# Performance work log

Measured on AMD Instinct MI355X. Metric: run time of the kernel, lower is better.

## Reference

```python
import jax, jax.numpy as jnp
import numpy as np

COST_CLASS = 1.0
COST_L1 = 1.0


def _lsa(cost):
    """Exact rectangular linear sum assignment (Jonker-Volgenant / e-maxx Hungarian).
    cost: (n, m) numpy float64 with n <= m. Returns ans[n]: column assigned to each row.
    """
    n, m = cost.shape
    INF = np.inf
    u = np.zeros(n + 1)
    v = np.zeros(m + 1)
    p = np.zeros(m + 1, dtype=np.int64)    # p[j]: 1-indexed row matched to column j (0 = free)
    way = np.zeros(m + 1, dtype=np.int64)
    for i in range(1, n + 1):
        p[0] = i
        j0 = 0
        minv = np.full(m + 1, INF)
        used = np.zeros(m + 1, dtype=bool)
        while True:
            used[j0] = True
            i0 = p[j0]
            minv1 = minv[1:]               # view, in-place updates propagate
            jmask = ~used[1:]
            cur = cost[i0 - 1, :] - u[i0] - v[1:]
            upd = jmask & (cur < minv1)
            minv1[upd] = cur[upd]
            way[1:][upd] = j0
            idx = np.nonzero(jmask)[0]
            j1rel = idx[np.argmin(minv1[idx])]
            delta = minv1[j1rel]
            u[p[used]] += delta
            v[used] -= delta
            minv1[jmask] -= delta
            j0 = j1rel + 1
            if p[j0] == 0:
                break
        # augment along the alternating path
        while j0:
            j1 = way[j0]
            p[j0] = p[j1]
            j0 = j1
    ans = np.zeros(n, dtype=np.int64)
    for j in range(1, m + 1):
        if p[j] > 0:
            ans[p[j] - 1] = j - 1
    return ans


def _solve_blocks(blocks):
    """blocks: (B, Q, T) numpy. Per-batch optimal assignment, scipy-compatible output:
    row_ind sorted ascending, min(Q,T) pairs (here Q >= T so T pairs)."""
    blocks = np.asarray(blocks, dtype=np.float64)
    B, Q, T = blocks.shape
    rows = np.empty((B, T), dtype=np.int32)
    cols = np.empty((B, T), dtype=np.int32)
    for b in range(B):
        c = blocks[b]
        if Q >= T:
            ans = _lsa(c.T)                      # ans[t] = matched query q
            order = np.argsort(ans, kind="stable")
            rows[b] = ans[order]
            cols[b] = order
        else:
            ans = _lsa(c)
            rows[b] = np.arange(Q)
            cols[b] = ans
    return rows, cols


def _cost_blocks(outputs, targets):
    """Diagonal (per-sample) blocks of the DETR cost matrix.
    outputs: (B, Q, 1+P); targets: (B, T, 1+P). Returns (B, Q, T).
    Math identical to building the full (B*Q, B*T) matrix and slicing, as in the source."""
    out_prob = jax.nn.softmax(outputs[:, :, 0], axis=-1)      # softmax over the QUERY axis (as in source)
    out_pos = outputs[:, :, 1:]                                # (B, Q, P)
    tgt_pos = targets[:, :, 1:]                                # (B, T, P)
    cost_l1 = jnp.abs(out_pos[:, :, None, :] - tgt_pos[:, None, :, :]).sum(-1)  # L1 cdist, (B, Q, T)
    return COST_CLASS * (-out_prob[:, :, None]) + COST_L1 * cost_l1


def setup_inputs() -> dict:
    key = jax.random.key(0)
    k1, k2 = jax.random.split(key)
    outputs = jax.random.normal(k1, (8, 2048, 3), dtype=jnp.float32)
    targets = jax.random.uniform(k2, (8, 256, 3), dtype=jnp.float32)
    return {"outputs": outputs, "targets": targets}


def reference(outputs, targets):
    blocks = _cost_blocks(outputs, targets)                    # (B, Q, T)
    B, Q, T = blocks.shape
    n = min(Q, T)
    shapes = (jax.ShapeDtypeStruct((B, n), jnp.int32),
              jax.ShapeDtypeStruct((B, n), jnp.int32))
    row_ind, col_ind = jax.pure_callback(_solve_blocks, shapes, blocks)
    return row_ind, col_ind
```

## Files before the change

### kernel.cpp

```cpp
#include <hip/hip_runtime.h>


constexpr int B = 8;
constexpr int Q = 2048;
constexpr int T = 256;
constexpr int NT = 256;
constexpr int KPT = Q / NT;
constexpr int NW = NT / 64;

struct __align__(16) CD { double u; float tx, ty; };

__device__ __forceinline__ unsigned wave_min_u32_dpp(unsigned a) {
  int v = (int)a, t;
  t = __builtin_amdgcn_update_dpp(v, v, 0x111, 0xf, 0xf, false);
  v = ((unsigned)t < (unsigned)v) ? t : v;
  t = __builtin_amdgcn_update_dpp(v, v, 0x112, 0xf, 0xf, false);
  v = ((unsigned)t < (unsigned)v) ? t : v;
  t = __builtin_amdgcn_update_dpp(v, v, 0x114, 0xf, 0xf, false);
  v = ((unsigned)t < (unsigned)v) ? t : v;
  t = __builtin_amdgcn_update_dpp(v, v, 0x118, 0xf, 0xf, false);
  v = ((unsigned)t < (unsigned)v) ? t : v;
  t = __builtin_amdgcn_update_dpp(v, v, 0x142, 0xf, 0xf, false);
  v = ((unsigned)t < (unsigned)v) ? t : v;
  t = __builtin_amdgcn_update_dpp(v, v, 0x143, 0xf, 0xf, false);
  v = ((unsigned)t < (unsigned)v) ? t : v;
  return (unsigned)__builtin_amdgcn_readlane(v, 63);
}

__launch_bounds__(NT, 1)
__global__ void hungarian_r14(const float* __restrict__ outs,
                              const float* __restrict__ tgts,
                              int* __restrict__ out) {
  const int b = blockIdx.x;
  const int tid = threadIdx.x;
  const int lane = tid & 63;
  const int wv = tid >> 6;

  __shared__ CD colDat[Q + 1];
  __shared__ float2 rowTgt[T + 1];
  __shared__ short p[Q + 1];
  __shared__ uint4 pk2[2][NW][2];
  __shared__ double vdelta[Q];
  __shared__ int ansArr[T];
  __shared__ double s_rv[NW];
  __shared__ float sh_f;

  const size_t qbase = (size_t)b * Q;
  const size_t tbase = (size_t)b * T;

  float xs[KPT], qx[KPT], qy[KPT];
#pragma unroll
  for (int k = 0; k < KPT; ++k) {
    const size_t o = (qbase + tid + k * NT) * 3;
    xs[k] = outs[o];
    qx[k] = outs[o + 1];
    qy[k] = outs[o + 2];
  }
  {
    const size_t o = (tbase + tid) * 3;
    rowTgt[tid + 1] = make_float2(tgts[o + 1], tgts[o + 2]);
    if (tid == 0) rowTgt[0] = make_float2(0.f, 0.f);
  }

  float lmax = xs[0];
#pragma unroll
  for (int k = 1; k < KPT; ++k) lmax = fmaxf(lmax, xs[k]);
  for (int off = 32; off > 0; off >>= 1) lmax = fmaxf(lmax, __shfl_down(lmax, off));
  if ((tid & 63) == 0) s_rv[tid >> 6] = (double)lmax;
  __syncthreads();
  if (tid == 0) {
    float m2 = (float)s_rv[0];
    for (int w = 1; w < NW; ++w) m2 = fmaxf(m2, (float)s_rv[w]);
    sh_f = m2;
  }
  __syncthreads();
  const float smax = sh_f;
  float ex[KPT];
  float lsum = 0.f;
#pragma unroll
  for (int k = 0; k < KPT; ++k) { ex[k] = expf(xs[k] - smax); lsum += ex[k]; }
  for (int off = 32; off > 0; off >>= 1) lsum += __shfl_down(lsum, off);
  if ((tid & 63) == 0) s_rv[tid >> 6] = (double)lsum;
  __syncthreads();
  if (tid == 0) {
    float s2 = 0.f;
    for (int w = 0; w < NW; ++w) s2 += (float)s_rv[w];
    sh_f = s2;
  }
  __syncthreads();
  const float ssum = sh_f;
  float np_[KPT];
#pragma unroll
  for (int k = 0; k < KPT; ++k) np_[k] = -(ex[k] / ssum);

  for (int j = tid; j <= Q; j += NT) {
    p[j] = 0;
    CD c0; c0.u = 0.0; c0.tx = -1.0f; c0.ty = 0.0f;
    colDat[j] = c0;
  }
  double vreg[KPT];
#pragma unroll
  for (int k = 0; k < KPT; ++k) {
    vreg[k] = 0.0;
    vdelta[tid + (k << 8)] = 0.0;
  }
  __syncthreads();

  const float FINF = __int_as_float(0x7f800000);
  float2 nxtT = rowTgt[1];

  for (int i = 1; i <= T; ++i) {
    unsigned usedMask = 0;
    double D = 0.0;
    int i0 = i;
    double ui0 = 0.0;
    float tX = nxtT.x, tY = nxtT.y;
    int s = 0, S;
    int j1v = 0;
    int recRow = 0, recCol = 0, recPrev = 0;
    double recU = 0.0, recD = 0.0;
    float recTX = 0.f, recTY = 0.f;

    for (;;) {
      if (tid == s) {
        recRow = i0; recU = ui0; recTX = tX; recTY = tY; recD = D; recPrev = j1v;
      }

      double cv[KPT];
#pragma unroll
      for (int k = 0; k < KPT; ++k) {
        float cf = fabsf(qx[k] - tX) + fabsf(qy[k] - tY) + np_[k];
        if (usedMask & (1u << k)) cf = FINF;
        cv[k] = ((double)cf - ui0) - vreg[k];
      }
      const double m01 = fmin(cv[0], cv[1]), m23 = fmin(cv[2], cv[3]);
      const double m45 = fmin(cv[4], cv[5]), m67 = fmin(cv[6], cv[7]);
      const double m03 = fmin(m01, m23), m47 = fmin(m45, m67);
      double bval = fmin(m03, m47);
      unsigned emsk = 0;
#pragma unroll
      for (int k = 0; k < KPT; ++k) emsk |= (cv[k] == bval) ? (1u << k) : 0u;
      const int bk = (int)__builtin_ctz(emsk);
      int bidx = 1 + tid + (bk << 8);

      const CD myCd = colDat[bidx];

      bval += 0.0;
      const long long bb = __double_as_longlong(bval);
      const unsigned long long key = (unsigned long long)bb ^
          ((bb < 0) ? 0xFFFFFFFFFFFFFFFFull : 0x8000000000000000ull);
      const unsigned khi = (unsigned)(key >> 32);
      const unsigned klo = (unsigned)key;

      const unsigned minhi = wave_min_u32_dpp(khi);
      const unsigned long long mask = __ballot(khi == minhi);
      int wl;
      if (__popcll(mask) == 1) {
        wl = (int)__ffsll(mask) - 1;
      } else {
        unsigned wklo = 0xffffffffu; int widx = 0x7fffffff; wl = 0;
        unsigned long long mm = mask;
        while (mm) {
          const int l = (int)__ffsll(mm) - 1; mm &= mm - 1;
          const unsigned lo2 = (unsigned)__builtin_amdgcn_readlane((int)klo, l);
          const int ix2 = __builtin_amdgcn_readlane(bidx, l);
          if (lo2 < wklo || (lo2 == wklo && ix2 < widx)) {
            wklo = lo2; widx = ix2; wl = l;
          }
        }
      }
      const int par = s & 1;
      if (lane == wl) {
        pk2[par][wv][0] = make_uint4(minhi, klo, (unsigned)bidx, 0u);
        const unsigned long long cu =
            (unsigned long long)__double_as_longlong(myCd.u);
        pk2[par][wv][1] = make_uint4((unsigned)cu, (unsigned)(cu >> 32),
                                     __float_as_uint(myCd.tx),
                                     __float_as_uint(myCd.ty));
      }
      __syncthreads();

      const uint4 c0v = pk2[par][0][0];
      const uint4 c1v = pk2[par][1][0];
      const uint4 c2v = pk2[par][2][0];
      const uint4 c3v = pk2[par][3][0];
      const uint4 d0v = pk2[par][0][1];
      const uint4 d1v = pk2[par][1][1];
      const uint4 d2v = pk2[par][2][1];
      const uint4 d3v = pk2[par][3][1];

      const unsigned long long k0b = ((unsigned long long)c0v.x << 32) | c0v.y;
      const unsigned long long k1b = ((unsigned long long)c1v.x << 32) | c1v.y;
      const unsigned long long k2b = ((unsigned long long)c2v.x << 32) | c2v.y;
      const unsigned long long k3b = ((unsigned long long)c3v.x << 32) | c3v.y;
      const int j0b = (int)c0v.z, j1bb = (int)c1v.z;
      const int j2b = (int)c2v.z, j3b = (int)c3v.z;
      const bool w01 = (k1b < k0b) || (k1b == k0b && j1bb < j0b);
      const unsigned long long k01 = w01 ? k1b : k0b;
      const int j01 = w01 ? j1bb : j0b;
      const bool w23 = (k3b < k2b) || (k3b == k2b && j3b < j2b);
      const unsigned long long k23 = w23 ? k3b : k2b;
      const int j23 = w23 ? j3b : j2b;
      const bool wf = (k23 < k01) || (k23 == k01 && j23 < j01);
      const unsigned long long bkk = wf ? k23 : k01;
      const int j1 = wf ? j23 : j01;
      const unsigned ulA = w01 ? d1v.x : d0v.x, uhA = w01 ? d1v.y : d0v.y;
      const unsigned xAf = w01 ? d1v.z : d0v.z, yAf = w01 ? d1v.w : d0v.w;
      const unsigned ulB = w23 ? d3v.x : d2v.x, uhB = w23 ? d3v.y : d2v.y;
      const unsigned xBf = w23 ? d3v.z : d2v.z, yBf = w23 ? d3v.w : d2v.w;
      const unsigned ulW = wf ? ulB : ulA, uhW = wf ? uhB : uhA;
      const unsigned xW = wf ? xBf : xAf, yW = wf ? yBf : yAf;
      const double cdun = __longlong_as_double(
          (long long)(((unsigned long long)uhW << 32) | ulW));
      const float cdtx = __uint_as_float(xW);
      const float cdty = __uint_as_float(yW);

      const long long db = (long long)((bkk & 0x8000000000000000ull)
                                           ? (bkk ^ 0x8000000000000000ull) : ~bkk);
      D += __longlong_as_double(db);
      if (tid == ((j1 - 1) & 255)) usedMask |= 1u << ((j1 - 1) >> 8);
      if (tid == s) recCol = j1;
      const int pj1 = (int)p[j1];
      j1v = j1;
      ++s;
      if (cdtx < 0.0f) { S = s; break; }
      ui0 = cdun; tX = cdtx; tY = cdty; i0 = pj1;
    }

    __syncthreads();
    nxtT = rowTgt[i < T ? i + 1 : T];
    const double Dfin = D;
    if (tid < S) {
      p[recCol] = (short)recRow;
      const double unew = recU + (Dfin - recD);
      CD c2; c2.u = unew; c2.tx = recTX; c2.ty = recTY;
      colDat[recCol] = c2;
      if (tid >= 1) {
        vdelta[recPrev - 1] = Dfin - recD;
      }
    }
    __syncthreads();
#pragma unroll
    for (int k = 0; k < KPT; ++k) {
      const double dv = vdelta[tid + (k << 8)];
      vreg[k] -= dv;
      vdelta[tid + (k << 8)] = 0.0;
    }
  }
  __syncthreads();

  for (int j = 1 + tid; j <= Q; j += NT) {
    const int pi = (int)p[j];
    if (pi > 0) ansArr[pi - 1] = j - 1;
  }
  __syncthreads();
  const int a = ansArr[tid];
  int rank = 0;
  for (int t2 = 0; t2 < T; ++t2) rank += (ansArr[t2] < a) ? 1 : 0;
  out[(size_t)b * T + rank] = a;
  out[(size_t)B * T + (size_t)b * T + rank] = tid;
}

extern "C" void kernel_launch(void* const* d_in, const int* in_sizes, int n_in,
                              void* d_out, int out_size, void* d_ws, size_t ws_size,
                              hipStream_t stream) {
  const float* outs = (const float*)d_in[0];
  const float* tgts = (const float*)d_in[1];
  int* out = (int*)d_out;
  hungarian_r14<<<B, NT, 0, stream>>>(outs, tgts, out);
}
```

Baseline: 864.6 us.

## Interleave two Hungarian solves per block to share barriers and hide latency

```diff
diff --git a/kernel.cpp b/kernel.cpp
--- a/kernel.cpp
+++ b/kernel.cpp
@@ -27,238 +27,296 @@
   return (unsigned)__builtin_amdgcn_readlane(v, 63);
 }
 
+struct CH {
+  float qx[KPT], qy[KPT], np_[KPT];
+  double vreg[KPT];
+  int i, mode;
+  unsigned usedMask;
+  double D, ui0;
+  float tX, tY;
+  int s, S, i0, j1v;
+  int recRow, recCol, recPrev;
+  double recU, recD;
+  float recTX, recTY;
+  int par, cpar;
+};
+
 __launch_bounds__(NT, 1)
-__global__ void hungarian_r14(const float* __restrict__ outs,
+__global__ void hungarian_r16(const float* __restrict__ outs,
                               const float* __restrict__ tgts,
                               int* __restrict__ out) {
-  const int b = blockIdx.x;
   const int tid = threadIdx.x;
   const int lane = tid & 63;
   const int wv = tid >> 6;
 
-  __shared__ CD colDat[Q + 1];
-  __shared__ float2 rowTgt[T + 1];
-  __shared__ short p[Q + 1];
-  __shared__ uint4 pk2[2][NW][2];
-  __shared__ double vdelta[Q];
-  __shared__ int ansArr[T];
+  __shared__ CD colDat[2][Q + 9];
+  __shared__ float2 rowTgt[2][T + 1];
+  __shared__ short p[2][Q + 1];
+  __shared__ uint4 pk2[2][2][NW][2];
+  __shared__ double vdelta[2][Q];
+  __shared__ int ansArr[2][T];
   __shared__ double s_rv[NW];
   __shared__ float sh_f;
 
-  const size_t qbase = (size_t)b * Q;
-  const size_t tbase = (size_t)b * T;
-
-  float xs[KPT], qx[KPT], qy[KPT];
-#pragma unroll
-  for (int k = 0; k < KPT; ++k) {
-    const size_t o = (qbase + tid + k * NT) * 3;
-    xs[k] = outs[o];
-    qx[k] = outs[o + 1];
-    qy[k] = outs[o + 2];
-  }
-  {
-    const size_t o = (tbase + tid) * 3;
-    rowTgt[tid + 1] = make_float2(tgts[o + 1], tgts[o + 2]);
-    if (tid == 0) rowTgt[0] = make_float2(0.f, 0.f);
-  }
-
-  float lmax = xs[0];
-#pragma unroll
-  for (int k = 1; k < KPT; ++k) lmax = fmaxf(lmax, xs[k]);
-  for (int off = 32; off > 0; off >>= 1) lmax = fmaxf(lmax, __shfl_down(lmax, off));
-  if ((tid & 63) == 0) s_rv[tid >> 6] = (double)lmax;
+  const float FINF = __int_as_float(0x7f800000);
+
+  CH cA, cB;
+
+  auto initChain = [&](CH& c, const int ci, const int bat) {
+    const size_t qbase = (size_t)bat * Q;
+    const size_t tbase = (size_t)bat * T;
+    float xs[KPT];
+#pragma unroll
+    for (int k = 0; k < KPT; ++k) {
+      const size_t o = (qbase + tid + k * NT) * 3;
+      xs[k] = outs[o];
+      c.qx[k] = outs[o + 1];
+      c.qy[k] = outs[o + 2];
+    }
+    {
+      const size_t o = (tbase + tid) * 3;
+      rowTgt[ci][tid + 1] = make_float2(tgts[o + 1], tgts[o + 2]);
+      if (tid == 0) rowTgt[ci][0] = make_float2(0.f, 0.f);
+    }
+    float lmax = xs[0];
+#pragma unroll
+    for (int k = 1; k < KPT; ++k) lmax = fmaxf(lmax, xs[k]);
+    for (int off = 32; off > 0; off >>= 1) lmax = fmaxf(lmax, __shfl_down(lmax, off));
+    if ((tid & 63) == 0) s_rv[tid >> 6] = (double)lmax;
+    __syncthreads();
+    if (tid == 0) {
+      float m2 = (float)s_rv[0];
+      for (int w = 1; w < NW; ++w) m2 = fmaxf(m2, (float)s_rv[w]);
+      sh_f = m2;
+    }
+    __syncthreads();
+    const float smax = sh_f;
+    float ex[KPT];
+    float lsum = 0.f;
+#pragma unroll
+    for (int k = 0; k < KPT; ++k) { ex[k] = expf(xs[k] - smax); lsum += ex[k]; }
+    for (int off = 32; off > 0; off >>= 1) lsum += __shfl_down(lsum, off);
+    if ((tid & 63) == 0) s_rv[tid >> 6] = (double)lsum;
+    __syncthreads();
+    if (tid == 0) {
+      float s2 = 0.f;
+      for (int w = 0; w < NW; ++w) s2 += (float)s_rv[w];
+      sh_f = s2;
+    }
+    __syncthreads();
+    const float ssum = sh_f;
+#pragma unroll
+    for (int k = 0; k < KPT; ++k) c.np_[k] = -(ex[k] / ssum);
+
+    for (int j = tid; j <= Q; j += NT) {
+      p[ci][j] = 0;
+      CD c0; c0.u = 0.0; c0.tx = -1.0f; c0.ty = 0.0f;
+      colDat[ci][j + (j >> 8)] = c0;
+    }
+#pragma unroll
+    for (int k = 0; k < KPT; ++k) {
+      c.vreg[k] = 0.0;
+      vdelta[ci][tid + (k << 8)] = 0.0;
+    }
+    c.par = 0; c.cpar = 0;
+    __syncthreads();
+    c.i = 1; c.mode = 0; c.usedMask = 0; c.D = 0.0; c.i0 = 1; c.ui0 = 0.0;
+    const float2 t0 = rowTgt[ci][1];
+    c.tX = t0.x; c.tY = t0.y;
+    c.s = 0; c.S = 0; c.j1v = 0;
+    c.recRow = 0; c.recCol = 0; c.recPrev = 0;
+    c.recU = 0.0; c.recD = 0.0; c.recTX = 0.f; c.recTY = 0.f;
+  };
+
+  auto advance_row = [&](CH& c, const int ci) {
+    c.i += 1;
+    if (c.i > T) { c.mode = 2; return; }
+    c.mode = 0;
+    c.usedMask = 0; c.D = 0.0; c.i0 = c.i; c.ui0 = 0.0;
+    const float2 tt = rowTgt[ci][c.i];
+    c.tX = tt.x; c.tY = tt.y;
+    c.s = 0; c.j1v = 0;
+  };
+
+  auto step_pre = [&](CH& c, const int ci) {
+    c.cpar = c.par; c.par ^= 1;
+    if (tid == c.s) {
+      c.recRow = c.i0; c.recU = c.ui0; c.recTX = c.tX; c.recTY = c.tY;
+      c.recD = c.D; c.recPrev = c.j1v;
+    }
+    double cv[KPT];
+#pragma unroll
+    for (int k = 0; k < KPT; ++k) {
+      float cf = fabsf(c.qx[k] - c.tX) + fabsf(c.qy[k] - c.tY) + c.np_[k];
+      if (c.usedMask & (1u << k)) cf = FINF;
+      cv[k] = ((double)cf - c.ui0) - c.vreg[k];
+    }
+    const double m01 = fmin(cv[0], cv[1]), m23 = fmin(cv[2], cv[3]);
+    const double m45 = fmin(cv[4], cv[5]), m67 = fmin(cv[6], cv[7]);
+    const double m03 = fmin(m01, m23), m47 = fmin(m45, m67);
+    double bval = fmin(m03, m47);
+    unsigned emsk = 0;
+#pragma unroll
+    for (int k = 0; k < KPT; ++k) emsk |= (cv[k] == bval) ? (1u << k) : 0u;
+    const int bk = (int)__builtin_ctz(emsk);
+    int bidx = 1 + tid + (bk << 8);
+
+    const CD myCd = colDat[ci][bidx + (bidx >> 8)];
+
+    bval += 0.0;
+    const long long bb = __double_as_longlong(bval);
+    const unsigned long long key = (unsigned long long)bb ^
+        ((bb < 0) ? 0xFFFFFFFFFFFFFFFFull : 0x8000000000000000ull);
+    const unsigned khi = (unsigned)(key >> 32);
+    const unsigned klo = (unsigned)key;
+
+    const unsigned minhi = wave_min_u32_dpp(khi);
+    const unsigned long long mask = __ballot(khi == minhi);
+    int wl;
+    if (__popcll(mask) == 1) {
+      wl = (int)__ffsll(mask) - 1;
+    } else {
+      unsigned wklo = 0xffffffffu; int widx = 0x7fffffff; wl = 0;
+      unsigned long long mm = mask;
+      while (mm) {
+        const int l = (int)__ffsll(mm) - 1; mm &= mm - 1;
+        const unsigned lo2 = (unsigned)__builtin_amdgcn_readlane((int)klo, l);
+        const int ix2 = __builtin_amdgcn_readlane(bidx, l);
+        if (lo2 < wklo || (lo2 == wklo && ix2 < widx)) {
+          wklo = lo2; widx = ix2; wl = l;
+        }
+      }
+    }
+    if (lane == wl) {
+      pk2[ci][c.cpar][wv][0] = make_uint4(minhi, klo, (unsigned)bidx, 0u);
+      const unsigned long long cu =
+          (unsigned long long)__double_as_longlong(myCd.u);
+      pk2[ci][c.cpar][wv][1] = make_uint4((unsigned)cu, (unsigned)(cu >> 32),
+                                          __float_as_uint(myCd.tx),
+                                          __float_as_uint(myCd.ty));
+    }
+  };
+
+  auto step_post = [&](CH& c, const int ci) {
+    const int cpar = c.cpar;
+    const uint4 c0v = pk2[ci][cpar][0][0];
+    const uint4 c1v = pk2[ci][cpar][1][0];
+    const uint4 c2v = pk2[ci][cpar][2][0];
+    const uint4 c3v = pk2[ci][cpar][3][0];
+    const uint4 d0v = pk2[ci][cpar][0][1];
+    const uint4 d1v = pk2[ci][cpar][1][1];
+    const uint4 d2v = pk2[ci][cpar][2][1];
+    const uint4 d3v = pk2[ci][cpar][3][1];
+
+    const unsigned long long k0b = ((unsigned long long)c0v.x << 32) | c0v.y;
+    const unsigned long long k1b = ((unsigned long long)c1v.x << 32) | c1v.y;
+    const unsigned long long k2b = ((unsigned long long)c2v.x << 32) | c2v.y;
+    const unsigned long long k3b = ((unsigned long long)c3v.x << 32) | c3v.y;
+    const int j0b = (int)c0v.z, j1bb = (int)c1v.z;
+    const int j2b = (int)c2v.z, j3b = (int)c3v.z;
+    const bool w01 = (k1b < k0b) || (k1b == k0b && j1bb < j0b);
+    const unsigned long long k01 = w01 ? k1b : k0b;
+    const int j01 = w01 ? j1bb : j0b;
+    const bool w23 = (k3b < k2b) || (k3b == k2b && j3b < j2b);
+    const unsigned long long k23 = w23 ? k3b : k2b;
+    const int j23 = w23 ? j3b : j2b;
+    const bool wf = (k23 < k01) || (k23 == k01 && j23 < j01);
+    const unsigned long long bkk = wf ? k23 : k01;
+    const int j1 = wf ? j23 : j01;
+    const unsigned ulA = w01 ? d1v.x : d0v.x, uhA = w01 ? d1v.y : d0v.y;
+    const unsigned xAf = w01 ? d1v.z : d0v.z, yAf = w01 ? d1v.w : d0v.w;
+    const unsigned ulB = w23 ? d3v.x : d2v.x, uhB = w23 ? d3v.y : d2v.y;
+    const unsigned xBf = w23 ? d3v.z : d2v.z, yBf = w23 ? d3v.w : d2v.w;
+    const unsigned ulW = wf ? ulB : ulA, uhW = wf ? uhB : uhA;
+    const unsigned xW = wf ? xBf : xAf, yW = wf ? yBf : yAf;
+    const double cdun = __longlong_as_double(
+        (long long)(((unsigned long long)uhW << 32) | ulW));
+    const float cdtx = __uint_as_float(xW);
+    const float cdty = __uint_as_float(yW);
+
+    const long long db = (long long)((bkk & 0x8000000000000000ull)
+                                         ? (bkk ^ 0x8000000000000000ull) : ~bkk);
+    c.D += __longlong_as_double(db);
+    if (tid == ((j1 - 1) & 255)) c.usedMask |= 1u << ((j1 - 1) >> 8);
+    if (tid == c.s) c.recCol = j1;
+    const int pj1 = (int)p[ci][j1];
+    c.j1v = j1;
+    ++c.s;
+    if (cdtx < 0.0f) {
+      c.S = c.s;
+      if (c.S == 1) {
+        const int jw = c.j1v;
+        if (tid == ((jw - 1) & 255)) {
+          p[ci][jw] = (short)c.i;
+          CD c2; c2.u = c.D; c2.tx = c.tX; c2.ty = c.tY;
+          colDat[ci][jw + (jw >> 8)] = c2;
+        }
+        advance_row(c, ci);
+      } else {
+        c.mode = 1;
+      }
+    } else {
+      c.ui0 = cdun; c.tX = cdtx; c.tY = cdty; c.i0 = pj1;
+    }
+  };
+
+  auto epi_scatter = [&](CH& c, const int ci) {
+    const double Dfin = c.D;
+    if (tid < c.S) {
+      p[ci][c.recCol] = (short)c.recRow;
+      const double unew = c.recU + (Dfin - c.recD);
+      CD c2; c2.u = unew; c2.tx = c.recTX; c2.ty = c.recTY;
+      colDat[ci][c.recCol + (c.recCol >> 8)] = c2;
+      if (tid >= 1) {
+        vdelta[ci][c.recPrev - 1] = Dfin - c.recD;
+      }
+    }
+  };
+
+  auto epi_apply = [&](CH& c, const int ci) {
+#pragma unroll
+    for (int k = 0; k < KPT; ++k) {
+      const double dv = vdelta[ci][tid + (k << 8)];
+      c.vreg[k] -= dv;
+      vdelta[ci][tid + (k << 8)] = 0.0;
+    }
+    advance_row(c, ci);
+  };
+
+  initChain(cA, 0, 2 * blockIdx.x);
+  initChain(cB, 1, 2 * blockIdx.x + 1);
   __syncthreads();
-  if (tid == 0) {
-    float m2 = (float)s_rv[0];
-    for (int w = 1; w < NW; ++w) m2 = fmaxf(m2, (float)s_rv[w]);
-    sh_f = m2;
+
+  while (cA.mode != 2 || cB.mode != 2) {
+    if (cA.mode == 0) step_pre(cA, 0);
+    else if (cA.mode == 1) epi_scatter(cA, 0);
+    if (cB.mode == 0) step_pre(cB, 1);
+    else if (cB.mode == 1) epi_scatter(cB, 1);
+    __syncthreads();
+    if (cA.mode == 0) step_post(cA, 0);
+    else if (cA.mode == 1) epi_apply(cA, 0);
+    if (cB.mode == 0) step_post(cB, 1);
+    else if (cB.mode == 1) epi_apply(cB, 1);
   }
   __syncthreads();
-  const float smax = sh_f;
-  float ex[KPT];
-  float lsum = 0.f;
-#pragma unroll
-  for (int k = 0; k < KPT; ++k) { ex[k] = expf(xs[k] - smax); lsum += ex[k]; }
-  for (int off = 32; off > 0; off >>= 1) lsum += __shfl_down(lsum, off);
-  if ((tid & 63) == 0) s_rv[tid >> 6] = (double)lsum;
-  __syncthreads();
-  if (tid == 0) {
-    float s2 = 0.f;
-    for (int w = 0; w < NW; ++w) s2 += (float)s_rv[w];
-    sh_f = s2;
+
+#pragma unroll
+  for (int ci = 0; ci < 2; ++ci) {
+    for (int j = 1 + tid; j <= Q; j += NT) {
+      const int pi = (int)p[ci][j];
+      if (pi > 0) ansArr[ci][pi - 1] = j - 1;
+    }
   }
   __syncthreads();
-  const float ssum = sh_f;
-  float np_[KPT];
-#pragma unroll
-  for (int k = 0; k < KPT; ++k) np_[k] = -(ex[k] / ssum);
-
-  for (int j = tid; j <= Q; j += NT) {
-    p[j] = 0;
-    CD c0; c0.u = 0.0; c0.tx = -1.0f; c0.ty = 0.0f;
-    colDat[j] = c0;
+#pragma unroll
+  for (int ci = 0; ci < 2; ++ci) {
+    const int bb = 2 * blockIdx.x + ci;
+    const int a = ansArr[ci][tid];
+    int rank = 0;
+    for (int t2 = 0; t2 < T; ++t2) rank += (ansArr[ci][t2] < a) ? 1 : 0;
+    out[(size_t)bb * T + rank] = a;
+    out[(size_t)B * T + (size_t)bb * T + rank] = tid;
   }
-  double vreg[KPT];
-#pragma unroll
-  for (int k = 0; k < KPT; ++k) {
-    vreg[k] = 0.0;
-    vdelta[tid + (k << 8)] = 0.0;
-  }
-  __syncthreads();
-
-  const float FINF = __int_as_float(0x7f800000);
-  float2 nxtT = rowTgt[1];
-
-  for (int i = 1; i <= T; ++i) {
-    unsigned usedMask = 0;
-    double D = 0.0;
-    int i0 = i;
-    double ui0 = 0.0;
-    float tX = nxtT.x, tY = nxtT.y;
-    int s = 0, S;
-    int j1v = 0;
-    int recRow = 0, recCol = 0, recPrev = 0;
-    double recU = 0.0, recD = 0.0;
-    float recTX = 0.f, recTY = 0.f;
-
-    for (;;) {
-      if (tid == s) {
-        recRow = i0; recU = ui0; recTX = tX; recTY = tY; recD = D; recPrev = j1v;
-      }
-
-      double cv[KPT];
-#pragma unroll
-      for (int k = 0; k < KPT; ++k) {
-        float cf = fabsf(qx[k] - tX) + fabsf(qy[k] - tY) + np_[k];
-        if (usedMask & (1u << k)) cf = FINF;
-        cv[k] = ((double)cf - ui0) - vreg[k];
-      }
-      const double m01 = fmin(cv[0], cv[1]), m23 = fmin(cv[2], cv[3]);
-      const double m45 = fmin(cv[4], cv[5]), m67 = fmin(cv[6], cv[7]);
-      const double m03 = fmin(m01, m23), m47 = fmin(m45, m67);
-      double bval = fmin(m03, m47);
-      unsigned emsk = 0;
-#pragma unroll
-      for (int k = 0; k < KPT; ++k) emsk |= (cv[k] == bval) ? (1u << k) : 0u;
-      const int bk = (int)__builtin_ctz(emsk);
-      int bidx = 1 + tid + (bk << 8);
-
-      const CD myCd = colDat[bidx];
-
-      bval += 0.0;
-      const long long bb = __double_as_longlong(bval);
-      const unsigned long long key = (unsigned long long)bb ^
-          ((bb < 0) ? 0xFFFFFFFFFFFFFFFFull : 0x8000000000000000ull);
-      const unsigned khi = (unsigned)(key >> 32);
-      const unsigned klo = (unsigned)key;
-
-      const unsigned minhi = wave_min_u32_dpp(khi);
-      const unsigned long long mask = __ballot(khi == minhi);
-      int wl;
-      if (__popcll(mask) == 1) {
-        wl = (int)__ffsll(mask) - 1;
-      } else {
-        unsigned wklo = 0xffffffffu; int widx = 0x7fffffff; wl = 0;
-        unsigned long long mm = mask;
-        while (mm) {
-          const int l = (int)__ffsll(mm) - 1; mm &= mm - 1;
-          const unsigned lo2 = (unsigned)__builtin_amdgcn_readlane((int)klo, l);
-          const int ix2 = __builtin_amdgcn_readlane(bidx, l);
-          if (lo2 < wklo || (lo2 == wklo && ix2 < widx)) {
-            wklo = lo2; widx = ix2; wl = l;
-          }
-        }
-      }
-      const int par = s & 1;
-      if (lane == wl) {
-        pk2[par][wv][0] = make_uint4(minhi, klo, (unsigned)bidx, 0u);
-        const unsigned long long cu =
-            (unsigned long long)__double_as_longlong(myCd.u);
-        pk2[par][wv][1] = make_uint4((unsigned)cu, (unsigned)(cu >> 32),
-                                     __float_as_uint(myCd.tx),
-                                     __float_as_uint(myCd.ty));
-      }
-      __syncthreads();
-
-      const uint4 c0v = pk2[par][0][0];
-      const uint4 c1v = pk2[par][1][0];
-      const uint4 c2v = pk2[par][2][0];
-      const uint4 c3v = pk2[par][3][0];
-      const uint4 d0v = pk2[par][0][1];
-      const uint4 d1v = pk2[par][1][1];
-      const uint4 d2v = pk2[par][2][1];
-      const uint4 d3v = pk2[par][3][1];
-
-      const unsigned long long k0b = ((unsigned long long)c0v.x << 32) | c0v.y;
-      const unsigned long long k1b = ((unsigned long long)c1v.x << 32) | c1v.y;
-      const unsigned long long k2b = ((unsigned long long)c2v.x << 32) | c2v.y;
-      const unsigned long long k3b = ((unsigned long long)c3v.x << 32) | c3v.y;
-      const int j0b = (int)c0v.z, j1bb = (int)c1v.z;
-      const int j2b = (int)c2v.z, j3b = (int)c3v.z;
-      const bool w01 = (k1b < k0b) || (k1b == k0b && j1bb < j0b);
-      const unsigned long long k01 = w01 ? k1b : k0b;
-      const int j01 = w01 ? j1bb : j0b;
-      const bool w23 = (k3b < k2b) || (k3b == k2b && j3b < j2b);
-      const unsigned long long k23 = w23 ? k3b : k2b;
-      const int j23 = w23 ? j3b : j2b;
-      const bool wf = (k23 < k01) || (k23 == k01 && j23 < j01);
-      const unsigned long long bkk = wf ? k23 : k01;
-      const int j1 = wf ? j23 : j01;
-      const unsigned ulA = w01 ? d1v.x : d0v.x, uhA = w01 ? d1v.y : d0v.y;
-      const unsigned xAf = w01 ? d1v.z : d0v.z, yAf = w01 ? d1v.w : d0v.w;
-      const unsigned ulB = w23 ? d3v.x : d2v.x, uhB = w23 ? d3v.y : d2v.y;
-      const unsigned xBf = w23 ? d3v.z : d2v.z, yBf = w23 ? d3v.w : d2v.w;
-      const unsigned ulW = wf ? ulB : ulA, uhW = wf ? uhB : uhA;
-      const unsigned xW = wf ? xBf : xAf, yW = wf ? yBf : yAf;
-      const double cdun = __longlong_as_double(
-          (long long)(((unsigned long long)uhW << 32) | ulW));
-      const float cdtx = __uint_as_float(xW);
-      const float cdty = __uint_as_float(yW);
-
-      const long long db = (long long)((bkk & 0x8000000000000000ull)
-                                           ? (bkk ^ 0x8000000000000000ull) : ~bkk);
-      D += __longlong_as_double(db);
-      if (tid == ((j1 - 1) & 255)) usedMask |= 1u << ((j1 - 1) >> 8);
-      if (tid == s) recCol = j1;
-      const int pj1 = (int)p[j1];
-      j1v = j1;
-      ++s;
-      if (cdtx < 0.0f) { S = s; break; }
-      ui0 = cdun; tX = cdtx; tY = cdty; i0 = pj1;
-    }
-
-    __syncthreads();
-    nxtT = rowTgt[i < T ? i + 1 : T];
-    const double Dfin = D;
-    if (tid < S) {
-      p[recCol] = (short)recRow;
-      const double unew = recU + (Dfin - recD);
-      CD c2; c2.u = unew; c2.tx = recTX; c2.ty = recTY;
-      colDat[recCol] = c2;
-      if (tid >= 1) {
-        vdelta[recPrev - 1] = Dfin - recD;
-      }
-    }
-    __syncthreads();
-#pragma unroll
-    for (int k = 0; k < KPT; ++k) {
-      const double dv = vdelta[tid + (k << 8)];
-      vreg[k] -= dv;
-      vdelta[tid + (k << 8)] = 0.0;
-    }
-  }
-  __syncthreads();
-
-  for (int j = 1 + tid; j <= Q; j += NT) {
-    const int pi = (int)p[j];
-    if (pi > 0) ansArr[pi - 1] = j - 1;
-  }
-  __syncthreads();
-  const int a = ansArr[tid];
-  int rank = 0;
-  for (int t2 = 0; t2 < T; ++t2) rank += (ansArr[t2] < a) ? 1 : 0;
-  out[(size_t)b * T + rank] = a;
-  out[(size_t)B * T + (size_t)b * T + rank] = tid;
 }
 
 extern "C" void kernel_launch(void* const* d_in, const int* in_sizes, int n_in,
@@ -267,5 +325,5 @@
   const float* outs = (const float*)d_in[0];
   const float* tgts = (const float*)d_in[1];
   int* out = (int*)d_out;
-  hungarian_r14<<<B, NT, 0, stream>>>(outs, tgts, out);
+  hungarian_r16<<<B / 2, NT, 0, stream>>>(outs, tgts, out);
 }
```

Result: slower. 1.720 ms (+99.0%).
